# Performance work log

Hardware: AMD Instinct MI355X
Metric: run time of the kernel (lower is better)

The kernel has to match this reference:

```python
import jax, jax.numpy as jnp
import numpy as np

B, L, D, H = 4, 1024, 1024, 16
HD = D // H            # head dim 64
MAXP = 1024            # max_position_embeddings
NADJ = 2               # teacher layers mapped to this student layer


def setup_inputs() -> dict:
    key = jax.random.key(0)
    ks = jax.random.split(key, 6)
    return {
        "hidden_states": jax.random.normal(ks[0], (B, L, D), jnp.float32),
        "attention_mask": jnp.zeros((B, 1, 1, L), jnp.float32),
        "teacher_w": jax.random.normal(ks[1], (3, NADJ, D, D), jnp.float32) * 0.02,
        "wl_w": jax.random.normal(ks[2], (3, NADJ), jnp.float32),
        "scale_w": jnp.ones((3, D, D), jnp.float32),
        "shift_w": jnp.zeros((3, D, D), jnp.float32),
        "teacher_b": jax.random.normal(ks[3], (3, NADJ, D), jnp.float32) * 0.02,
        "wl_b": jax.random.normal(ks[4], (3, NADJ), jnp.float32),
        "scale_b": jnp.ones((3, D), jnp.float32),
        "shift_b": jnp.zeros((3, D), jnp.float32),
        "dist_emb": jax.random.normal(ks[5], (2 * MAXP - 1, HD), jnp.float32) * 0.02,
    }


def reference(hidden_states, attention_mask, teacher_w, wl_w, scale_w, shift_w,
              teacher_b, wl_b, scale_b, shift_b, dist_emb):
    # Teacher-distilled weight/bias generation (WeightGenerator/BiasGenerator):
    # student = tanh(mode-0 contraction of teacher subset with W_l) * W + B
    w = jnp.tanh(jnp.einsum('pl,ploi->poi', wl_w, teacher_w)) * scale_w + shift_w  # [3,out,in]
    b = jnp.tanh(jnp.einsum('pl,plo->po', wl_b, teacher_b)) * scale_b + shift_b    # [3,out]

    def proj(i):
        y = jnp.einsum('bld,od->blo', hidden_states, w[i]) + b[i]
        return y.reshape(B, L, H, HD).transpose(0, 2, 1, 3)  # [B,H,L,HD]

    q, k, v = proj(0), proj(1), proj(2)

    scores = jnp.einsum('bhld,bhrd->bhlr', q, k)  # [B,H,L,L]

    # relative_key_query positional bias
    dist = jnp.arange(L)[:, None] - jnp.arange(L)[None, :] + (MAXP - 1)  # [L,L]
    pe = dist_emb[dist]                                                  # [L,L,HD]
    scores = scores \
        + jnp.einsum('bhld,lrd->bhlr', q, pe) \
        + jnp.einsum('bhrd,lrd->bhlr', k, pe)

    scores = scores / np.sqrt(HD).astype(np.float32) + attention_mask
    probs = jax.nn.softmax(scores, axis=-1)  # dropout p=0.0 (eval)

    ctx = jnp.einsum('bhlr,bhrd->bhld', probs, v)
    return ctx.transpose(0, 2, 1, 3).reshape(B, L, D)
```

## Files before the change

### kernel.cpp

```cpp
#include <hip/hip_runtime.h>
#include <hip/hip_bf16.h>
#include <math.h>

#define D_  1024
#define L_  1024
#define B_  4
#define H_  16
#define HD_ 64

typedef __attribute__((ext_vector_type(4))) short short4_t;
typedef __attribute__((ext_vector_type(8))) short short8_t;
typedef __attribute__((ext_vector_type(4))) float f4;
typedef unsigned short u16;

__device__ __forceinline__ f4 MF(short8_t a, short8_t b, f4 c) {
  return __builtin_amdgcn_mfma_f32_16x16x32_bf16(a, b, c, 0, 0, 0);
}
__device__ __forceinline__ unsigned fbits(float x) { return __builtin_bit_cast(unsigned, x); }
__device__ __forceinline__ float bf2f(unsigned short u) {
  return __builtin_bit_cast(float, (unsigned)u << 16);
}
__device__ __forceinline__ unsigned pack2hi(float x, float y) {
  return (fbits(x) >> 16) | (fbits(y) & 0xFFFF0000u);
}
__device__ __forceinline__ float bfres(float x) {
  return x - __builtin_bit_cast(float, fbits(x) & 0xFFFF0000u);
}
__device__ __forceinline__ void gload16(const void* g, void* l) {
  __builtin_amdgcn_global_load_lds(
      (const __attribute__((address_space(1))) unsigned*)g,
      (__attribute__((address_space(3))) unsigned*)l, 16, 0, 0);
}
__device__ __forceinline__ short8_t ldsfragP(const char* base, int row, int ci) {
  return *(const short8_t*)(base + row * 128 + ((ci ^ (row & 7)) << 4));
}
__device__ __forceinline__ int perm32(int c) {
  return (c & ~31) | (((c >> 2) & 3) << 3) | (((c >> 4) & 1) << 2);
}

__global__ __launch_bounds__(256) void wgen_kernel(
    const float* __restrict__ tw, const float* __restrict__ wl,
    const float* __restrict__ sc, const float* __restrict__ sh,
    u16* __restrict__ whi, u16* __restrict__ wlo) {
  size_t i4 = (size_t)blockIdx.x * 256 + threadIdx.x;
  size_t e = i4 * 4;
  int p = (int)(e >> 20);
  size_t rem = e & 0xFFFFFu;
  float a0 = wl[p * 2 + 0], a1 = wl[p * 2 + 1];
  float4 t0 = *(const float4*)&tw[((size_t)(p * 2 + 0) << 20) + rem];
  float4 t1 = *(const float4*)&tw[((size_t)(p * 2 + 1) << 20) + rem];
  float4 s4 = *(const float4*)&sc[e];
  float4 h4 = *(const float4*)&sh[e];
  float4 o;
  o.x = tanhf(a0 * t0.x + a1 * t1.x) * s4.x + h4.x;
  o.y = tanhf(a0 * t0.y + a1 * t1.y) * s4.y + h4.y;
  o.z = tanhf(a0 * t0.z + a1 * t1.z) * s4.z + h4.z;
  o.w = tanhf(a0 * t0.w + a1 * t1.w) * s4.w + h4.w;
  const size_t off = (e & ~(size_t)1023) + perm32((int)(e & 1023) & 31) +
                     (((int)(e & 1023)) & ~31);
  uint2 hi; hi.x = pack2hi(o.x, o.y); hi.y = pack2hi(o.z, o.w);
  *(uint2*)&whi[off] = hi;
  uint2 lo; lo.x = pack2hi(bfres(o.x), bfres(o.y)); lo.y = pack2hi(bfres(o.z), bfres(o.w));
  *(uint2*)&wlo[off] = lo;
}

__global__ __launch_bounds__(256) void bgen_kernel(
    const float* __restrict__ tb, const float* __restrict__ wl,
    const float* __restrict__ sc, const float* __restrict__ sh,
    float* __restrict__ b_out) {
  int i = blockIdx.x * 256 + threadIdx.x;
  int p = i >> 10;
  int o = i & 1023;
  float v = tanhf(wl[p * 2 + 0] * tb[(p * 2 + 0) * D_ + o] +
                  wl[p * 2 + 1] * tb[(p * 2 + 1) * D_ + o]);
  b_out[i] = v * sc[i] + sh[i];
}

__global__ __launch_bounds__(256) void ecvt_kernel(
    const float* __restrict__ emb, u16* __restrict__ embh) {
  int i4 = blockIdx.x * 256 + threadIdx.x;
  if (i4 >= 32752) return;
  int e = i4 * 4;
  float4 v = *(const float4*)&emb[e];
  uint2 h2; h2.x = pack2hi(v.x, v.y); h2.y = pack2hi(v.z, v.w);
  int pe = (e & ~31) | perm32(e & 31);
  *(uint2*)&embh[pe] = h2;
}

__global__ __launch_bounds__(256) void proj_mfma_kernel(
    const float* __restrict__ hs,
    const u16* __restrict__ Bhp, const u16* __restrict__ Blp,
    const float* __restrict__ bias,
    u16* __restrict__ Qhi, u16* __restrict__ Qlo,
    u16* __restrict__ Khi, u16* __restrict__ Klo,
    u16* __restrict__ Vthi, u16* __restrict__ Vtlo) {
  __shared__ u16 Ah[128][32], Al[128][32], Bh[128][32], Bl[128][32];
  const int tid  = threadIdx.x;
  const int lane = tid & 63;
  const int wv   = tid >> 6;
  const int wm   = wv >> 1, wn = wv & 1;
  const int l15  = lane & 15, g = lane >> 4;

  const int bid = (blockIdx.x & 7) * 96 + (blockIdx.x >> 3);
  const int mt = bid & 31, nt = bid >> 5;
  const int m0 = mt * 128, n0 = nt * 128;

  f4 acc[4][4];
#pragma unroll
  for (int i = 0; i < 4; ++i)
#pragma unroll
    for (int j = 0; j < 4; ++j) acc[i][j] = f4{0.f, 0.f, 0.f, 0.f};

#pragma unroll 1
  for (int k0 = 0; k0 < D_; k0 += 32) {
#pragma unroll
    for (int s = 0; s < 4; ++s) {
      int q = wv * 4 + s;
      int plane = q >> 3, rowg = q & 7;
      const u16* src = (plane ? Blp : Bhp) +
                       (size_t)(n0 + rowg * 16 + (lane >> 2)) * 1024 + k0 + (lane & 3) * 8;
      u16* dst = (plane ? &Bl[0][0] : &Bh[0][0]) + rowg * 512;
      gload16(src, dst);
    }
#pragma unroll
    for (int c = 0; c < 4; ++c) {
      int f4id = tid + c * 256;
      int row = f4id >> 3, q4 = f4id & 7;
      float4 v = *(const float4*)&hs[(size_t)(m0 + row) * 1024 + k0 + q4 * 4];
      int col = (q4 & 3) * 8 + ((q4 >> 2) & 1) * 4;
      uint2 hi2; hi2.x = pack2hi(v.x, v.y); hi2.y = pack2hi(v.z, v.w);
      *(uint2*)&Ah[row][col] = hi2;
      uint2 lo2; lo2.x = pack2hi(bfres(v.x), bfres(v.y)); lo2.y = pack2hi(bfres(v.z), bfres(v.w));
      *(uint2*)&Al[row][col] = lo2;
    }
    __syncthreads();

    short8_t ah[4], al[4], bh[4], bl[4];
#pragma unroll
    for (int i = 0; i < 4; ++i) {
      ah[i] = *(const short8_t*)&Ah[wm * 64 + i * 16 + l15][g * 8];
      al[i] = *(const short8_t*)&Al[wm * 64 + i * 16 + l15][g * 8];
      bh[i] = *(const short8_t*)&Bh[wn * 64 + i * 16 + l15][g * 8];
      bl[i] = *(const short8_t*)&Bl[wn * 64 + i * 16 + l15][g * 8];
    }
#pragma unroll
    for (int mi = 0; mi < 4; ++mi)
#pragma unroll
      for (int ni = 0; ni < 4; ++ni) {
        acc[mi][ni] = MF(ah[mi], bh[ni], acc[mi][ni]);
        acc[mi][ni] = MF(ah[mi], bl[ni], acc[mi][ni]);
        acc[mi][ni] = MF(al[mi], bh[ni], acc[mi][ni]);
      }
    __syncthreads();
  }

  const int p = n0 >> 10;
  const int h0 = (n0 >> 6) & 15;
  const int nbase = n0 + wn * 64;
  float bnv[4];
#pragma unroll
  for (int ni = 0; ni < 4; ++ni) bnv[ni] = bias[nbase + ni * 16 + l15];
  float* T = (float*)&Ah[0][0];

#pragma unroll
  for (int mi = 0; mi < 4; ++mi) {
    __syncthreads();
#pragma unroll
    for (int ni = 0; ni < 4; ++ni)
#pragma unroll
      for (int r = 0; r < 4; ++r)
        T[(wm * 16 + 4 * g + r) * 132 + wn * 64 + ni * 16 + l15] =
            acc[mi][ni][r] + bnv[ni];
    __syncthreads();

    if (p < 2) {
      u16* PH = p ? Khi : Qhi;
      u16* PL = p ? Klo : Qlo;
      const int lr = tid >> 3;
      const int m = m0 + (lr >> 4) * 64 + mi * 16 + (lr & 15);
      const int bb = m >> 10, l = m & 1023;
#pragma unroll
      for (int c = 0; c < 4; ++c) {
        const int col = 4 * (tid & 7) + 32 * c;
        const int pc = perm32(col & 63) | (col & 64);
        const int hd = pc & 63, hl = col >> 6;
        float4 v = *(const float4*)&T[lr * 132 + col];
        uint2 hi; hi.x = pack2hi(v.x, v.y); hi.y = pack2hi(v.z, v.w);
        uint2 lo; lo.x = pack2hi(bfres(v.x), bfres(v.y)); lo.y = pack2hi(bfres(v.z), bfres(v.w));
        const size_t ad = ((size_t)(bb * 16 + h0 + hl) << 16) + (size_t)l * 64 + hd;
        *(uint2*)&PH[ad] = hi;
        *(uint2*)&PL[ad] = lo;
      }
    } else {
      const int col = (tid >> 3) & 31;
#pragma unroll
      for (int c = 0; c < 4; ++c) {
        const int cc = col + 32 * c;
        const int hd = cc & 63, hl = cc >> 6;
        const int mq = tid & 7;
        const int lr0 = 4 * mq;
        float vv[4];
#pragma unroll
        for (int k = 0; k < 4; ++k) vv[k] = T[(lr0 + k) * 132 + cc];
        const int m = m0 + (lr0 >> 4) * 64 + mi * 16 + (lr0 & 15);
        const int bb = m >> 10, l = m & 1023;
        const int pl = (l & ~31) | perm32(l & 31);
        uint2 hi; hi.x = pack2hi(vv[0], vv[1]); hi.y = pack2hi(vv[2], vv[3]);
        uint2 lo; lo.x = pack2hi(bfres(vv[0]), bfres(vv[1]));
        lo.y = pack2hi(bfres(vv[2]), bfres(vv[3]));
        const size_t ad = ((size_t)(bb * 16 + h0 + hl) << 16) + (size_t)hd * 1024 + pl;
        *(uint2*)&Vthi[ad] = hi;
        *(uint2*)&Vtlo[ad] = lo;
      }
    }
  }
}

#define KD_OFF 0
#define VD_OFF 32768
#define ER_OFF 49152
#define UB_OFF 81920
#define WB_OFF 115712
#define SM4_SIZE 149504

__global__ __launch_bounds__(512, 2) void attn6_kernel(
    const u16* __restrict__ Qhi, const u16* __restrict__ Qlo,
    const u16* __restrict__ Khi, const u16* __restrict__ Klo,
    const u16* __restrict__ Vthi, const u16* __restrict__ Vtlo,
    const u16* __restrict__ embh, const float* __restrict__ mask,
    float* __restrict__ out) {
  __shared__ __align__(16) char sm[SM4_SIZE];
  char* ERb = sm + ER_OFF;

  const int tid  = threadIdx.x;
  const int lane = tid & 63;
  const int wv   = tid >> 6;
  const int t    = wv >> 2;
  const int lh   = (wv >> 1) & 1;
  const int rh   = wv & 1;
  const int l15  = lane & 15;
  const int g    = lane >> 4;
  const int rsub = lane >> 3;
  const int scol = ((lane & 7) ^ (lane >> 3)) << 3;

  const int bid = (blockIdx.x & 7) * 64 + (blockIdx.x >> 3);
  const int lp = bid & 7, h = (bid >> 3) & 15, b = bid >> 7;
  const int l0 = lp * 128;
  const size_t bhoff = (size_t)(b * 16 + h) << 16;
  const float* maskp = mask + b * L_;

  u16* UBt = (u16*)(sm + UB_OFF) + t * 8448;
  u16* WBt = (u16*)(sm + WB_OFF) + t * 8448;

#pragma unroll
  for (int s = 0; s < 4; ++s) {
    const int idx = wv * 4 + s;
    const int plane = idx >> 4, rowg = idx & 15;
    const u16* src = (plane ? Qlo : Qhi) + bhoff +
                     (size_t)(l0 + rowg * 8 + rsub) * 64 + scol;
    gload16(src, ERb + (plane * 16 + rowg) * 1024);
  }
  __syncthreads();

  short8_t qfh[2][2], qfl[2][2];
#pragma unroll
  for (int nb = 0; nb < 2; ++nb)
#pragma unroll
    for (int kc = 0; kc < 2; ++kc) {
      const int row = 64 * t + 32 * lh + 16 * nb + l15;
      qfh[nb][kc] = ldsfragP(ERb,         row, 4 * kc + g);
      qfl[nb][kc] = ldsfragP(ERb + 16384, row, 4 * kc + g);
    }
  __syncthreads();

  {
#pragma unroll
    for (int s = 0; s < 2; ++s) {
      const int idx = wv * 2 + s;
      const int plane = idx >> 3, rowg = idx & 7;
      const u16* ks = (plane ? Klo : Khi) + bhoff +
                      (size_t)(rowg * 8 + rsub) * 64 + scol;
      gload16(ks, sm + KD_OFF + plane * 8192 + rowg * 1024);
    }
    const int dmin0 = l0 + 960;
#pragma unroll
    for (int s = 0; s < 3; ++s) {
      const int grp = wv * 3 + s;
      const int slot = (dmin0 + grp * 8) & 255;
      gload16(embh + (size_t)(dmin0 + grp * 8 + rsub) * 64 + scol,
              ERb + slot * 128);
    }
  }

  f4 o_acc[4][2];
#pragma unroll
  for (int i = 0; i < 4; ++i)
#pragma unroll
    for (int j = 0; j < 2; ++j) o_acc[i][j] = f4{0.f, 0.f, 0.f, 0.f};
  float mrun[2] = {-3e38f, -3e38f};
  float lsum[2] = {0.f, 0.f};

#pragma unroll 1
  for (int rt = 0; rt < 16; ++rt) {
    const int r0 = rt * 64;
    const int cur = rt & 1;
    const int dmin = l0 - r0 + 960;

    __syncthreads();

    if (rt < 15) {
      char* kdn = sm + KD_OFF + (cur ^ 1) * 16384;
#pragma unroll
      for (int s = 0; s < 2; ++s) {
        const int idx = wv * 2 + s;
        const int plane = idx >> 3, rowg = idx & 7;
        const u16* ks = (plane ? Klo : Khi) + bhoff +
                        (size_t)(r0 + 64 + rowg * 8 + rsub) * 64 + scol;
        gload16(ks, kdn + plane * 8192 + rowg * 1024);
      }
      const int rowE = dmin - 64 + wv * 8;
      const int slot = rowE & 255;
      gload16(embh + (size_t)(rowE + rsub) * 64 + scol, ERb + slot * 128);
    }
#pragma unroll
    for (int s = 0; s < 2; ++s) {
      const int idx = wv * 2 + s;
      const int plane = idx >> 3, rowg = idx & 7;
      const u16* vs = (plane ? Vtlo : Vthi) + bhoff +
                      (size_t)(rowg * 8 + rsub) * 1024 + r0 + scol;
      gload16(vs, sm + VD_OFF + plane * 8192 + rowg * 1024);
    }

    float4 mk[2];
#pragma unroll
    for (int mb = 0; mb < 2; ++mb)
      mk[mb] = *(const float4*)&maskp[r0 + 32 * rh + 16 * mb + 4 * g];

    const char* kdc_h = sm + KD_OFF + cur * 16384;
    const char* kdc_l = kdc_h + 8192;

    f4 sacc[2][2];
#pragma unroll
    for (int i = 0; i < 2; ++i)
#pragma unroll
      for (int j = 0; j < 2; ++j) sacc[i][j] = f4{0.f, 0.f, 0.f, 0.f};
    short8_t khf[2][2];
#pragma unroll
    for (int mb = 0; mb < 2; ++mb)
#pragma unroll
      for (int kc = 0; kc < 2; ++kc) {
        const int row = 32 * rh + 16 * mb + l15;
        short8_t ka = ldsfragP(kdc_h, row, 4 * kc + g);
        short8_t kl = ldsfragP(kdc_l, row, 4 * kc + g);
        khf[mb][kc] = ka;
#pragma unroll
        for (int nb = 0; nb < 2; ++nb) {
          sacc[mb][nb] = MF(ka, qfh[nb][kc], sacc[mb][nb]);
          sacc[mb][nb] = MF(ka, qfl[nb][kc], sacc[mb][nb]);
          sacc[mb][nb] = MF(kl, qfh[nb][kc], sacc[mb][nb]);
        }
      }

#pragma unroll
    for (int s = 0; s < 3; ++s) {
      const int dblk = 16 * (2 * lh + 3 * rh + s);
      const int erow = (dmin + 64 * t + dblk + l15) & 255;
      const short8_t eb0 = ldsfragP(ERb, erow, g);
      const short8_t eb1 = ldsfragP(ERb, erow, 4 + g);
      f4 au0 = f4{0.f, 0.f, 0.f, 0.f}, au1 = f4{0.f, 0.f, 0.f, 0.f};
      au0 = MF(eb0, qfh[0][0], au0); au0 = MF(eb1, qfh[0][1], au0);
      au1 = MF(eb0, qfh[1][0], au1); au1 = MF(eb1, qfh[1][1], au1);
#pragma unroll
      for (int nb = 0; nb < 2; ++nb) {
        const f4 au = nb ? au1 : au0;
        uint2 w2; w2.x = pack2hi(au[0], au[1]); w2.y = pack2hi(au[2], au[3]);
        *(uint2*)&UBt[(32 * lh + 16 * nb + l15) * 132 + dblk + 4 * g] = w2;
      }
    }

#pragma unroll
    for (int s = 0; s < 3; ++s) {
      const int dblk = 16 * ((2 - 2 * rh) + 3 * lh + s);
      const int erow = (dmin + 64 * t + dblk + l15) & 255;
      const short8_t eb0 = ldsfragP(ERb, erow, g);
      const short8_t eb1 = ldsfragP(ERb, erow, 4 + g);
      f4 aw0 = f4{0.f, 0.f, 0.f, 0.f}, aw1 = f4{0.f, 0.f, 0.f, 0.f};
      aw0 = MF(eb0, khf[0][0], aw0); aw0 = MF(eb1, khf[0][1], aw0);
      aw1 = MF(eb0, khf[1][0], aw1); aw1 = MF(eb1, khf[1][1], aw1);
#pragma unroll
      for (int mb = 0; mb < 2; ++mb) {
        const f4 aw = mb ? aw1 : aw0;
        uint2 w2; w2.x = pack2hi(aw[0], aw[1]); w2.y = pack2hi(aw[2], aw[3]);
        *(uint2*)&WBt[(32 * rh + 16 * mb + l15) * 132 + dblk + 4 * g] = w2;
      }
    }
    __syncthreads();

    float pbuf[2][2][4];
#pragma unroll
    for (int nb = 0; nb < 2; ++nb) {
      const int lA = 32 * lh + 16 * nb + l15;
      float sv[2][4];
      float ml = -3e38f;
#pragma unroll
      for (int mb = 0; mb < 2; ++mb) {
        const int rr = 32 * rh + 16 * mb + 4 * g;
        const int dbase = lA + 63 - rr;
        const float mka[4] = {mk[mb].x, mk[mb].y, mk[mb].z, mk[mb].w};
#pragma unroll
        for (int j = 0; j < 4; ++j) {
          const float uu = bf2f(UBt[lA * 132 + dbase - j]);
          const float ww = bf2f(WBt[(rr + j) * 132 + dbase - j]);
          float s = (sacc[mb][nb][j] + uu + ww) * 0.125f + mka[j];
          sv[mb][j] = s;
          ml = fmaxf(ml, s);
        }
      }
      ml = fmaxf(ml, __shfl_xor(ml, 16));
      ml = fmaxf(ml, __shfl_xor(ml, 32));
      const float mn = fmaxf(mrun[nb], ml);
      const float rs = __expf(mrun[nb] - mn);
      float ps = 0.f;
#pragma unroll
      for (int mb = 0; mb < 2; ++mb)
#pragma unroll
        for (int j = 0; j < 4; ++j) {
          const float pv = __expf(sv[mb][j] - mn);
          pbuf[nb][mb][j] = pv;
          ps += pv;
        }
      ps += __shfl_xor(ps, 16);
      ps += __shfl_xor(ps, 32);
      lsum[nb] = lsum[nb] * rs + ps;
      mrun[nb] = mn;
#pragma unroll
      for (int mbd = 0; mbd < 4; ++mbd) {
        o_acc[mbd][nb][0] *= rs; o_acc[mbd][nb][1] *= rs;
        o_acc[mbd][nb][2] *= rs; o_acc[mbd][nb][3] *= rs;
      }
    }

    short8_t pf[2], pl_[2];
#pragma unroll
    for (int nb = 0; nb < 2; ++nb) {
      union { unsigned u[4]; short8_t v; } uh, ul;
      uh.u[0] = pack2hi(pbuf[nb][0][0], pbuf[nb][0][1]);
      uh.u[1] = pack2hi(pbuf[nb][0][2], pbuf[nb][0][3]);
      uh.u[2] = pack2hi(pbuf[nb][1][0], pbuf[nb][1][1]);
      uh.u[3] = pack2hi(pbuf[nb][1][2], pbuf[nb][1][3]);
      pf[nb] = uh.v;
      ul.u[0] = pack2hi(bfres(pbuf[nb][0][0]), bfres(pbuf[nb][0][1]));
      ul.u[1] = pack2hi(bfres(pbuf[nb][0][2]), bfres(pbuf[nb][0][3]));
      ul.u[2] = pack2hi(bfres(pbuf[nb][1][0]), bfres(pbuf[nb][1][1]));
      ul.u[3] = pack2hi(bfres(pbuf[nb][1][2]), bfres(pbuf[nb][1][3]));
      pl_[nb] = ul.v;
    }
    const char* vdc_h = sm + VD_OFF;
    const char* vdc_l = vdc_h + 8192;
#pragma unroll
    for (int mbd = 0; mbd < 4; ++mbd) {
      short8_t vh = ldsfragP(vdc_h, 16 * mbd + l15, 4 * rh + g);
      short8_t vl = ldsfragP(vdc_l, 16 * mbd + l15, 4 * rh + g);
#pragma unroll
      for (int nb = 0; nb < 2; ++nb) {
        o_acc[mbd][nb] = MF(vh, pf[nb], o_acc[mbd][nb]);
        o_acc[mbd][nb] = MF(vh, pl_[nb], o_acc[mbd][nb]);
        o_acc[mbd][nb] = MF(vl, pf[nb], o_acc[mbd][nb]);
      }
    }
  }

  __syncthreads();
  float* mbuf = (float*)ERb;
  float* obuf = (float*)(sm + UB_OFF);
  if (g == 0) {
#pragma unroll
    for (int nb = 0; nb < 2; ++nb) {
      mbuf[((wv * 2 + nb) * 16 + l15) * 2 + 0] = mrun[nb];
      mbuf[((wv * 2 + nb) * 16 + l15) * 2 + 1] = lsum[nb];
    }
  }
  __syncthreads();
  const int pw = wv ^ 1;
  float alpha[2], ltot[2];
#pragma unroll
  for (int nb = 0; nb < 2; ++nb) {
    float m2 = mbuf[((pw * 2 + nb) * 16 + l15) * 2 + 0];
    float s2 = mbuf[((pw * 2 + nb) * 16 + l15) * 2 + 1];
    float M = fmaxf(mrun[nb], m2);
    alpha[nb] = __expf(mrun[nb] - M);
    ltot[nb] = lsum[nb] * alpha[nb] + s2 * __expf(m2 - M);
  }
  const int pair = wv >> 1;
  if (rh == 1) {
#pragma unroll
    for (int mbd = 0; mbd < 4; ++mbd)
#pragma unroll
      for (int nb = 0; nb < 2; ++nb)
#pragma unroll
        for (int j = 0; j < 4; ++j)
          obuf[(pair * 64 + 16 * mbd + 4 * g + j) * 32 + 16 * nb + l15] =
              o_acc[mbd][nb][j] * alpha[nb];
  }
  __syncthreads();
  if (rh == 0) {
#pragma unroll
    for (int mbd = 0; mbd < 4; ++mbd)
#pragma unroll
      for (int nb = 0; nb < 2; ++nb) {
        const int lgl = l0 + 64 * t + 32 * lh + 16 * nb + l15;
        const float inv = 1.f / ltot[nb];
        float tmp[4];
#pragma unroll
        for (int j = 0; j < 4; ++j)
          tmp[j] = (o_acc[mbd][nb][j] * alpha[nb] +
                    obuf[(pair * 64 + 16 * mbd + 4 * g + j) * 32 + 16 * nb + l15]) * inv;
        float4 ov; ov.x = tmp[0]; ov.y = tmp[1]; ov.z = tmp[2]; ov.w = tmp[3];
        *(float4*)&out[(size_t)(b * L_ + lgl) * D_ + h * HD_ + 16 * mbd + 4 * g] = ov;
      }
  }
}

extern "C" void kernel_launch(void* const* d_in, const int* in_sizes, int n_in,
                              void* d_out, int out_size, void* d_ws, size_t ws_size,
                              hipStream_t stream) {
  const float* hs   = (const float*)d_in[0];
  const float* mask = (const float*)d_in[1];
  const float* tw   = (const float*)d_in[2];
  const float* wlw  = (const float*)d_in[3];
  const float* scw  = (const float*)d_in[4];
  const float* shw  = (const float*)d_in[5];
  const float* tb   = (const float*)d_in[6];
  const float* wlb  = (const float*)d_in[7];
  const float* scb  = (const float*)d_in[8];
  const float* shb  = (const float*)d_in[9];
  const float* emb  = (const float*)d_in[10];
  float* out = (float*)d_out;

  char* W = (char*)d_ws;
  float* b_s = (float*)W;
  u16* whi  = (u16*)(W + 12288);
  u16* wlo  = whi + 3145728;
  u16* embh = wlo + 3145728;
  u16* Qhi  = embh + 131072;
  u16* Qlo  = Qhi + 4194304;
  u16* Khi  = Qlo + 4194304;
  u16* Klo  = Khi + 4194304;
  u16* Vthi = Klo + 4194304;
  u16* Vtlo = Vthi + 4194304;

  hipLaunchKernelGGL(wgen_kernel, dim3(3072), dim3(256), 0, stream,
                     tw, wlw, scw, shw, whi, wlo);
  hipLaunchKernelGGL(bgen_kernel, dim3(12), dim3(256), 0, stream,
                     tb, wlb, scb, shb, b_s);
  hipLaunchKernelGGL(ecvt_kernel, dim3(128), dim3(256), 0, stream, emb, embh);
  hipLaunchKernelGGL(proj_mfma_kernel, dim3(768), dim3(256), 0, stream,
                     hs, whi, wlo, b_s, Qhi, Qlo, Khi, Klo, Vthi, Vtlo);
  hipLaunchKernelGGL(attn6_kernel, dim3(512), dim3(512), 0, stream,
                     Qhi, Qlo, Khi, Klo, Vthi, Vtlo, embh, mask, out);
}
```

Measured before the change: 249.8 us.

## Hoist load pointers, unroll loop, add MFMA priority, skip unneeded softmax rescale

The attention kernel now precomputes the global K/V/embedding source pointers and LDS destinations once and advances them by fixed strides, instead of recomputing addresses every iteration. The tile loop is unrolled by two. s_setprio raises wave priority around the QK and PV MFMA blocks. The online softmax skips the exp and accumulator rescale when no lane's row max increases (checked with a wave-wide vote). These changes aim to cut scalar/VALU overhead; the risks are higher register pressure from the unroll and a divergent branch.

New measurement: 250.4 us. About the same (+0.3%).

```diff
diff --git a/kernel.cpp b/kernel.cpp
--- a/kernel.cpp
+++ b/kernel.cpp
@@ -223,7 +223,7 @@
 #define WB_OFF 115712
 #define SM4_SIZE 149504
 
-__global__ __launch_bounds__(512, 2) void attn6_kernel(
+__global__ __launch_bounds__(512, 2) void attn7_kernel(
     const u16* __restrict__ Qhi, const u16* __restrict__ Qlo,
     const u16* __restrict__ Khi, const u16* __restrict__ Klo,
     const u16* __restrict__ Vthi, const u16* __restrict__ Vtlo,
@@ -273,15 +273,23 @@
     }
   __syncthreads();
 
+  const int pl0 = (wv * 2 + 0) >> 3, rg0 = (wv * 2 + 0) & 7;
+  const int pl1 = (wv * 2 + 1) >> 3, rg1 = (wv * 2 + 1) & 7;
+  const u16* kb0 = (pl0 ? Klo : Khi) + bhoff + (size_t)(rg0 * 8 + rsub) * 64 + scol;
+  const u16* kb1 = (pl1 ? Klo : Khi) + bhoff + (size_t)(rg1 * 8 + rsub) * 64 + scol;
+  const u16* vp0 = (pl0 ? Vtlo : Vthi) + bhoff + (size_t)(rg0 * 8 + rsub) * 1024 + scol;
+  const u16* vp1 = (pl1 ? Vtlo : Vthi) + bhoff + (size_t)(rg1 * 8 + rsub) * 1024 + scol;
+  const u16* ep  = embh + (size_t)(l0 + 896 + wv * 8 + rsub) * 64 + scol;
+  const u16* kp0 = kb0 + 4096;
+  const u16* kp1 = kb1 + 4096;
+  char* const kdst0 = sm + KD_OFF + pl0 * 8192 + rg0 * 1024;
+  char* const kdst1 = sm + KD_OFF + pl1 * 8192 + rg1 * 1024;
+  char* const vdst0 = sm + VD_OFF + pl0 * 8192 + rg0 * 1024;
+  char* const vdst1 = sm + VD_OFF + pl1 * 8192 + rg1 * 1024;
+
   {
-#pragma unroll
-    for (int s = 0; s < 2; ++s) {
-      const int idx = wv * 2 + s;
-      const int plane = idx >> 3, rowg = idx & 7;
-      const u16* ks = (plane ? Klo : Khi) + bhoff +
-                      (size_t)(rowg * 8 + rsub) * 64 + scol;
-      gload16(ks, sm + KD_OFF + plane * 8192 + rowg * 1024);
-    }
+    gload16(kb0, kdst0);
+    gload16(kb1, kdst1);
     const int dmin0 = l0 + 960;
 #pragma unroll
     for (int s = 0; s < 3; ++s) {
@@ -300,7 +308,7 @@
   float mrun[2] = {-3e38f, -3e38f};
   float lsum[2] = {0.f, 0.f};
 
-#pragma unroll 1
+#pragma unroll 2
   for (int rt = 0; rt < 16; ++rt) {
     const int r0 = rt * 64;
     const int cur = rt & 1;
@@ -310,26 +318,16 @@
 
     if (rt < 15) {
       char* kdn = sm + KD_OFF + (cur ^ 1) * 16384;
-#pragma unroll
-      for (int s = 0; s < 2; ++s) {
-        const int idx = wv * 2 + s;
-        const int plane = idx >> 3, rowg = idx & 7;
-        const u16* ks = (plane ? Klo : Khi) + bhoff +
-                        (size_t)(r0 + 64 + rowg * 8 + rsub) * 64 + scol;
-        gload16(ks, kdn + plane * 8192 + rowg * 1024);
-      }
-      const int rowE = dmin - 64 + wv * 8;
-      const int slot = rowE & 255;
-      gload16(embh + (size_t)(rowE + rsub) * 64 + scol, ERb + slot * 128);
-    }
-#pragma unroll
-    for (int s = 0; s < 2; ++s) {
-      const int idx = wv * 2 + s;
-      const int plane = idx >> 3, rowg = idx & 7;
-      const u16* vs = (plane ? Vtlo : Vthi) + bhoff +
-                      (size_t)(rowg * 8 + rsub) * 1024 + r0 + scol;
-      gload16(vs, sm + VD_OFF + plane * 8192 + rowg * 1024);
-    }
+      gload16(kp0, kdn + pl0 * 8192 + rg0 * 1024);
+      gload16(kp1, kdn + pl1 * 8192 + rg1 * 1024);
+      kp0 += 4096; kp1 += 4096;
+      const int slot = (dmin - 64 + wv * 8) & 255;
+      gload16(ep, ERb + slot * 128);
+      ep -= 4096;
+    }
+    gload16(vp0, vdst0);
+    gload16(vp1, vdst1);
+    vp0 += 64; vp1 += 64;
 
     float4 mk[2];
 #pragma unroll
@@ -345,6 +343,7 @@
 #pragma unroll
       for (int j = 0; j < 2; ++j) sacc[i][j] = f4{0.f, 0.f, 0.f, 0.f};
     short8_t khf[2][2];
+    __builtin_amdgcn_s_setprio(1);
 #pragma unroll
     for (int mb = 0; mb < 2; ++mb)
 #pragma unroll
@@ -360,6 +359,7 @@
           sacc[mb][nb] = MF(kl, qfh[nb][kc], sacc[mb][nb]);
         }
       }
+    __builtin_amdgcn_s_setprio(0);
 
 #pragma unroll
     for (int s = 0; s < 3; ++s) {
@@ -418,8 +418,8 @@
       }
       ml = fmaxf(ml, __shfl_xor(ml, 16));
       ml = fmaxf(ml, __shfl_xor(ml, 32));
-      const float mn = fmaxf(mrun[nb], ml);
-      const float rs = __expf(mrun[nb] - mn);
+      const bool nore = __all(ml <= mrun[nb]);
+      const float mn = nore ? mrun[nb] : fmaxf(mrun[nb], ml);
       float ps = 0.f;
 #pragma unroll
       for (int mb = 0; mb < 2; ++mb)
@@ -431,12 +431,17 @@
         }
       ps += __shfl_xor(ps, 16);
       ps += __shfl_xor(ps, 32);
-      lsum[nb] = lsum[nb] * rs + ps;
-      mrun[nb] = mn;
-#pragma unroll
-      for (int mbd = 0; mbd < 4; ++mbd) {
-        o_acc[mbd][nb][0] *= rs; o_acc[mbd][nb][1] *= rs;
-        o_acc[mbd][nb][2] *= rs; o_acc[mbd][nb][3] *= rs;
+      if (nore) {
+        lsum[nb] += ps;
+      } else {
+        const float rs = __expf(mrun[nb] - mn);
+        lsum[nb] = lsum[nb] * rs + ps;
+        mrun[nb] = mn;
+#pragma unroll
+        for (int mbd = 0; mbd < 4; ++mbd) {
+          o_acc[mbd][nb][0] *= rs; o_acc[mbd][nb][1] *= rs;
+          o_acc[mbd][nb][2] *= rs; o_acc[mbd][nb][3] *= rs;
+        }
       }
     }
 
@@ -457,6 +462,7 @@
     }
     const char* vdc_h = sm + VD_OFF;
     const char* vdc_l = vdc_h + 8192;
+    __builtin_amdgcn_s_setprio(1);
 #pragma unroll
     for (int mbd = 0; mbd < 4; ++mbd) {
       short8_t vh = ldsfragP(vdc_h, 16 * mbd + l15, 4 * rh + g);
@@ -468,6 +474,7 @@
         o_acc[mbd][nb] = MF(vl, pf[nb], o_acc[mbd][nb]);
       }
     }
+    __builtin_amdgcn_s_setprio(0);
   }
 
   __syncthreads();
@@ -556,6 +563,6 @@
   hipLaunchKernelGGL(ecvt_kernel, dim3(128), dim3(256), 0, stream, emb, embh);
   hipLaunchKernelGGL(proj_mfma_kernel, dim3(768), dim3(256), 0, stream,
                      hs, whi, wlo, b_s, Qhi, Qlo, Khi, Klo, Vthi, Vtlo);
-  hipLaunchKernelGGL(attn6_kernel, dim3(512), dim3(512), 0, stream,
+  hipLaunchKernelGGL(attn7_kernel, dim3(512), dim3(512), 0, stream,
                      Qhi, Qlo, Khi, Klo, Vthi, Vtlo, embh, mask, out);
 }
```
